# Optimization experiments

Measured on AMD Instinct MI355X. Metric: run time of the kernel, lower is better.

Reference implementation:

```python
import jax, jax.numpy as jnp
import numpy as np

BATCH, SEQ, DIM, DSTATE = 8, 2048, 1024, 16


def setup_inputs() -> dict:
    key = jax.random.key(0)
    ks = jax.random.split(key, 8)
    u = jax.random.normal(ks[0], (BATCH, SEQ, DIM), jnp.float32)
    gate = jax.random.normal(ks[1], (BATCH, SEQ, DIM), jnp.float32)
    # parameters (init per module: normal std=0.01 for A_log/B/C, zeros for D)
    A_log = 0.01 * jax.random.normal(ks[2], (DSTATE, DSTATE), jnp.float32)
    B_mat = 0.01 * jax.random.normal(ks[3], (DIM, DSTATE), jnp.float32)
    C_mat = 0.01 * jax.random.normal(ks[4], (DIM, DSTATE), jnp.float32)
    D = jnp.zeros((DIM,), jnp.float32)
    bound = 1.0 / np.sqrt(DIM)  # nn.Linear default init
    dt_w = jax.random.uniform(ks[5], (1, DIM), jnp.float32, -bound, bound)
    dt_b = jax.random.uniform(ks[6], (1,), jnp.float32, -bound, bound)
    return {"u": u, "gate": gate, "A_log": A_log, "B_mat": B_mat,
            "C_mat": C_mat, "D": D, "dt_w": dt_w, "dt_b": dt_b}


def reference(u, gate, A_log, B_mat, C_mat, D, dt_w, dt_b):
    # delta = sigmoid(Linear(gate)) : [B, S, 1] -> [B, S]
    delta = jax.nn.sigmoid(jnp.einsum('bsd,od->bso', gate, dt_w) + dt_b)[..., 0]
    A = -jnp.exp(A_log)                               # [N, N]
    scaled_A = delta[..., None, None] * A             # [B, S, N, N]
    A_exp = jax.scipy.linalg.expm(scaled_A)           # batched matrix exp
    Bu = jnp.einsum('bsd,dn->bsn', u, B_mat)          # [B, S, N]

    def step(h, inp):
        Aexp_t, bu_t = inp                            # [B,N,N], [B,N]
        h = jnp.einsum('bn,bnm->bm', h, Aexp_t) + bu_t
        return h, h

    h0 = jnp.zeros((u.shape[0], DSTATE), u.dtype)
    _, hs = jax.lax.scan(step, h0, (jnp.swapaxes(A_exp, 0, 1), jnp.swapaxes(Bu, 0, 1)))
    hs = jnp.swapaxes(hs, 0, 1)                       # [B, S, N]
    y = jnp.einsum('bsn,dn->bsd', hs, C_mat) + D * u  # [B, S, D]
    return y
```

## Files before the change

kernel.cpp:

```cpp
#include <hip/hip_runtime.h>

#define BATCH  8
#define SEQ    2048
#define DIMSZ  1024
#define NST    16
#define LCH    32
#define CPB    (SEQ / LCH)
#define NCHUNK (BATCH * CPB)
#define NCHEB  32
#define PI_F   3.14159265358979f

typedef __attribute__((ext_vector_type(8))) short bf16x8;
typedef __attribute__((ext_vector_type(4))) float f32x4;

static __device__ __forceinline__ unsigned short f2bf(float f) {
    unsigned u = __builtin_bit_cast(unsigned, f);
    unsigned r = (u + 0x7FFFu + ((u >> 16) & 1u)) >> 16;
    return (unsigned short)r;
}
static __device__ __forceinline__ float bf2f(unsigned short h) {
    unsigned u = ((unsigned)h) << 16;
    return __builtin_bit_cast(float, u);
}

__global__ __launch_bounds__(256) void sA_nodes(
    const float* __restrict__ A_log, float* __restrict__ Fn)
{
    __shared__ float Xs[16 * 17];
    __shared__ float Ts[16 * 17];
    const int tid = threadIdx.x;
    const int i = tid >> 4, j = tid & 15;
    const float th = (2.f * blockIdx.x + 1.f) * (PI_F / 64.f);
    const float dl = 0.5f * (1.f + cosf(th));
    const float a  = -expf(A_log[tid]);
    const float x  = dl * a * (1.0f / 64.0f);
    Xs[i*17 + j] = x;
    Ts[i*17 + j] = x;
    float S = x + (i == j ? 1.0f : 0.0f);
    __syncthreads();
#pragma unroll
    for (int k = 2; k <= 8; ++k) {
        float nt = 0.f;
#pragma unroll
        for (int kk = 0; kk < 16; ++kk)
            nt = fmaf(Ts[i*17 + kk], Xs[kk*17 + j], nt);
        nt *= (1.0f / (float)k);
        S += nt;
        __syncthreads();
        Ts[i*17 + j] = nt;
        __syncthreads();
    }
#pragma unroll
    for (int r = 0; r < 6; ++r) {
        __syncthreads();
        Ts[i*17 + j] = S;
        __syncthreads();
        float nt = 0.f;
#pragma unroll
        for (int kk = 0; kk < 16; ++kk)
            nt = fmaf(Ts[i*17 + kk], Ts[kk*17 + j], nt);
        S = nt;
    }
    Fn[(size_t)blockIdx.x * 256 + tid] = S;
}

__global__ __launch_bounds__(256) void sB_setup(
    const float* __restrict__ Fn, const float* __restrict__ B_mat,
    float* __restrict__ Gt,
    unsigned short* __restrict__ Bfh, unsigned short* __restrict__ Bfl)
{
    const int tid = threadIdx.x;
    const int blk = blockIdx.x;
    if (blk < NCHEB) {
        const int m = blk;
        float acc = 0.f;
        for (int k = 0; k < NCHEB; ++k) {
            const float th = (2.f * k + 1.f) * (PI_F / 64.f);
            acc = fmaf(Fn[(size_t)k * 256 + tid], cosf(m * th), acc);
        }
        const float sc = (m == 0) ? (1.f / 32.f) : (2.f / 32.f);
        Gt[(size_t)tid * NCHEB + m] = acc * sc;
    } else {
        const int idx0 = (blk - NCHEB) * 2048;
        for (int t = 0; t < 8; ++t) {
            const int idx = idx0 + t * 256 + tid;
            const int j  = idx & 7;
            const int l  = (idx >> 3) & 63;
            const int ks = idx >> 9;
            const int k  = ks * 32 + ((l >> 4) << 3) + j;
            const int n  = l & 15;
            float bv = B_mat[(size_t)k * 16 + n];
            unsigned short h = f2bf(bv);
            Bfh[idx] = h;
            Bfl[idx] = f2bf(bv - bf2f(h));
        }
    }
}

__global__ __launch_bounds__(256) void k1a_delta(
    const float* __restrict__ gate, const float* __restrict__ dt_w,
    const float* __restrict__ dt_b, float* __restrict__ delta)
{
    const int tid  = threadIdx.x;
    const int lane = tid & 63;
    const int w    = tid >> 6;
    const int tok  = blockIdx.x * 4 + w;
    const float* gp = gate + (size_t)tok * DIMSZ;
    float s = 0.f;
#pragma unroll
    for (int i = 0; i < 4; ++i) {
        const float4 g  = *(const float4*)(gp   + i * 256 + lane * 4);
        const float4 wv = *(const float4*)(dt_w + i * 256 + lane * 4);
        s = fmaf(g.x, wv.x, s); s = fmaf(g.y, wv.y, s);
        s = fmaf(g.z, wv.z, s); s = fmaf(g.w, wv.w, s);
    }
#pragma unroll
    for (int off = 32; off >= 1; off >>= 1)
        s += __shfl_xor(s, off, 64);
    if (lane == 0)
        delta[tok] = 1.0f / (1.0f + expf(-(s + dt_b[0])));
}

__global__ __launch_bounds__(512, 4) void kBA2(
    const float* __restrict__ u,
    const unsigned short* __restrict__ Bfh, const unsigned short* __restrict__ Bfl,
    const float* __restrict__ Gt, const float* __restrict__ delta,
    float* __restrict__ Bu, float* __restrict__ P, float* __restrict__ e)
{
    __shared__ float smem[12288];
    __shared__ float Bus[LCH * NST];
    __shared__ float dl[LCH];
    __shared__ float sd[1];
    __shared__ float Ps[16 * 17];
    const int tid  = threadIdx.x;
    const int lane = tid & 63;
    const int w    = tid >> 6;
    const size_t gI = blockIdx.x;
    const int tok0 = (int)gI * 32;
    const int qk   = w & 3;
    const int wrow = (w >> 2) * 16;
    const int q    = lane >> 4;
    const int r    = lane & 15;

    if (tid < LCH) dl[tid] = delta[gI * LCH + tid];

    const uint4* bh = (const uint4*)Bfh;
    const uint4* bl = (const uint4*)Bfl;

    const int srow = 4 * w + (lane >> 5);
    const int p    = lane & 31;
    int colb[2];
#pragma unroll
    for (int i = 0; i < 2; ++i) {
        const int row = srow + 2 * i;
        colb[i] = 256 * (p >> 3) + 4 * ((p & 7) ^ (row & 7));
    }

    auto stage = [&](int c, int b) {
#pragma unroll
        for (int i = 0; i < 2; ++i) {
            const float* gp = u + (size_t)(tok0 + srow + 2 * i) * DIMSZ
                                + (colb[i] + c * 32);
            __builtin_amdgcn_global_load_lds(
                (const __attribute__((address_space(1))) void*)gp,
                (__attribute__((address_space(3))) void*)&smem[b * 4096 + (4 * w + 2 * i) * 128],
                16, 0, 0);
        }
    };

    f32x4 acc = {0.f, 0.f, 0.f, 0.f};
    uint4 fh[2], fl[2];

    fh[0] = bh[(qk * 8 + 0) * 64 + lane];
    fl[0] = bl[(qk * 8 + 0) * 64 + lane];
    stage(0, 0);
    stage(1, 1);
    stage(2, 2);
    asm volatile("s_waitcnt vmcnt(4)" ::: "memory");
    __builtin_amdgcn_sched_barrier(0);
    __builtin_amdgcn_s_barrier();

#pragma unroll
    for (int c = 0; c < 8; ++c) {
        const int b = c % 3;
        float fu[8];
        {
            const int c0 = qk * 8 + ((2 * q + 0) ^ (r & 7));
            const int c1 = qk * 8 + ((2 * q + 1) ^ (r & 7));
            const float4 v0 = *(const float4*)&smem[b * 4096 + (wrow + r) * 128 + c0 * 4];
            const float4 v1 = *(const float4*)&smem[b * 4096 + (wrow + r) * 128 + c1 * 4];
            fu[0] = v0.x; fu[1] = v0.y; fu[2] = v0.z; fu[3] = v0.w;
            fu[4] = v1.x; fu[5] = v1.y; fu[6] = v1.z; fu[7] = v1.w;
        }
        asm volatile("s_waitcnt lgkmcnt(0)" ::: "memory");
        __builtin_amdgcn_sched_barrier(0);
        __builtin_amdgcn_s_barrier();
        if (c + 1 < 8) {
            const int ks = qk * 8 + c + 1;
            fh[(c + 1) & 1] = bh[ks * 64 + lane];
            fl[(c + 1) & 1] = bl[ks * 64 + lane];
        }
        if (c + 3 < 8) stage(c + 3, (c + 3) % 3);
        __builtin_amdgcn_sched_barrier(0);
        {
            bf16x8 uh, ul;
#pragma unroll
            for (int i = 0; i < 8; ++i) {
                unsigned short h = f2bf(fu[i]);
                uh[i] = (short)h;
                ul[i] = (short)f2bf(fu[i] - bf2f(h));
            }
            const bf16x8 Bh = __builtin_bit_cast(bf16x8, fh[c & 1]);
            const bf16x8 Bl = __builtin_bit_cast(bf16x8, fl[c & 1]);
            acc = __builtin_amdgcn_mfma_f32_16x16x32_bf16(uh, Bh, acc, 0, 0, 0);
            acc = __builtin_amdgcn_mfma_f32_16x16x32_bf16(uh, Bl, acc, 0, 0, 0);
            acc = __builtin_amdgcn_mfma_f32_16x16x32_bf16(ul, Bh, acc, 0, 0, 0);
        }
        if (c < 7) {
            if (c == 6) asm volatile("s_waitcnt vmcnt(4)" ::: "memory");
            else        asm volatile("s_waitcnt vmcnt(6)" ::: "memory");
            __builtin_amdgcn_sched_barrier(0);
            __builtin_amdgcn_s_barrier();
        }
    }

    float* red = smem;
#pragma unroll
    for (int rr = 0; rr < 4; ++rr)
        red[w * 256 + (q * 4 + rr) * 16 + r] = acc[rr];
    __syncthreads();
    float bv;
    if (tid < 256) bv = red[tid]       + red[256 + tid] + red[512 + tid]  + red[768 + tid];
    else           bv = red[768 + tid] + red[1024 + tid] + red[1280 + tid] + red[1536 + tid];
    Bu[gI * 512 + tid] = bv;
    Bus[tid] = bv;

    const int el = tid & 255;
    float gr[NCHEB];
    {
        const float4* gp = (const float4*)(Gt + (size_t)el * NCHEB);
#pragma unroll
        for (int qq = 0; qq < NCHEB / 4; ++qq) {
            float4 v = gp[qq];
            gr[qq*4+0] = v.x; gr[qq*4+1] = v.y; gr[qq*4+2] = v.z; gr[qq*4+3] = v.w;
        }
    }
    __syncthreads();
    if (tid == 0) {
        float s = 0.f;
        for (int t = 0; t < LCH; ++t) s += dl[t];
        sd[0] = s;
    }
    const int tgrp = tid >> 8;
    for (int t = tgrp * 16; t < tgrp * 16 + 16; ++t) {
        const float x = 2.f * dl[t] - 1.f;
        float accm = fmaf(gr[1], x, gr[0]);
        float tm2 = 1.f, tm1 = x;
#pragma unroll
        for (int m = 2; m < NCHEB; ++m) {
            const float tm = fmaf(2.f * x, tm1, -tm2);
            accm = fmaf(gr[m], tm, accm);
            tm2 = tm1; tm1 = tm;
        }
        smem[t * 272 + (el >> 4) * 17 + (el & 15)] = accm;
    }
    __syncthreads();
    float S;
    {
        const float xp = 2.f * (sd[0] * (1.f / LCH)) - 1.f;
        float accm = fmaf(gr[1], xp, gr[0]);
        float tm2 = 1.f, tm1 = xp;
#pragma unroll
        for (int m = 2; m < NCHEB; ++m) {
            const float tm = fmaf(2.f * xp, tm1, -tm2);
            accm = fmaf(gr[m], tm, accm);
            tm2 = tm1; tm1 = tm;
        }
        S = accm;
    }
    const int i = el >> 4, j = el & 15;
#pragma unroll
    for (int rr = 0; rr < 5; ++rr) {
        if (tid < 256) Ps[i*17 + j] = S;
        __syncthreads();
        float ns = 0.f;
#pragma unroll
        for (int k = 0; k < 16; ++k)
            ns = fmaf(Ps[i*17 + k], Ps[k*17 + j], ns);
        __syncthreads();
        S = ns;
    }
    if (tid < 256) P[gI * 256 + tid] = S;
    if (tid < 64) {
        const int gq = tid >> 4, jj = tid & 15, i0 = gq * 4;
        float h = 0.f;
        for (int t = 0; t < LCH; ++t) {
            float pp = 0.f;
#pragma unroll
            for (int m = 0; m < 4; ++m)
                pp = fmaf(__shfl(h, gq * 20 + m, 64),
                          smem[t * 272 + (i0 + m) * 17 + jj], pp);
            pp += __shfl_xor(pp, 16, 64);
            pp += __shfl_xor(pp, 32, 64);
            h = Bus[t * 16 + jj] + pp;
        }
        if (gq == 0) e[gI * NST + jj] = h;
    }
}

__global__ __launch_bounds__(256) void k4_scan(
    const float* __restrict__ P, const float* __restrict__ e,
    float* __restrict__ hin)
{
    __shared__ float Pl[32 * 272];
    __shared__ float el[32 * NST];
    const int tid = threadIdx.x;
    const int b = blockIdx.x;
    float h = 0.f;
    for (int half = 0; half < 2; ++half) {
        const int c0 = half * 32;
        for (int idx = tid; idx < 32*256; idx += 256) {
            const int c = idx >> 8, ij = idx & 255, i = ij >> 4, jj = ij & 15;
            Pl[c*272 + i*17 + jj] = P[((size_t)(b*CPB + c0 + c)) * 256 + ij];
        }
        for (int idx = tid; idx < 32*NST; idx += 256)
            el[idx] = e[((size_t)(b*CPB + c0)) * NST + idx];
        __syncthreads();
        if (tid < 64) {
            const int gq = tid >> 4, j = tid & 15, i0 = gq * 4;
            for (int c = 0; c < 32; ++c) {
                if (tid < 16) hin[((size_t)(b*CPB + c0 + c)) * NST + j] = h;
                float pp = 0.f;
#pragma unroll
                for (int m = 0; m < 4; ++m)
                    pp = fmaf(__shfl(h, gq * 20 + m, 64),
                              Pl[c*272 + (i0 + m)*17 + j], pp);
                pp += __shfl_xor(pp, 16, 64);
                pp += __shfl_xor(pp, 32, 64);
                h = el[c*16 + j] + pp;
            }
        }
        __syncthreads();
    }
}

__global__ __launch_bounds__(512, 4) void k5b(
    const float* __restrict__ Gt, const float* __restrict__ delta,
    const float* __restrict__ Bu, const float* __restrict__ hin,
    const float* __restrict__ u, const float* __restrict__ C_mat,
    const float* __restrict__ D, float* __restrict__ y)
{
    __shared__ float Mlds[32 * 272];
    __shared__ float Bus[LCH * NST];
    __shared__ float dl[LCH];
    __shared__ __align__(16) float Hs[LCH * NST];
    const int tid = threadIdx.x;
    const size_t g = blockIdx.x;
    const int el = tid & 255;
    const int tgrp = tid >> 8;
    if (tid < LCH) dl[tid] = delta[g * LCH + tid];
    Bus[tid] = Bu[g * 512 + tid];
    float gr[NCHEB];
    {
        const float4* gp = (const float4*)(Gt + (size_t)el * NCHEB);
#pragma unroll
        for (int qq = 0; qq < NCHEB / 4; ++qq) {
            float4 v = gp[qq];
            gr[qq*4+0] = v.x; gr[qq*4+1] = v.y; gr[qq*4+2] = v.z; gr[qq*4+3] = v.w;
        }
    }
    __syncthreads();
    for (int t = tgrp * 16; t < tgrp * 16 + 16; ++t) {
        const float x = 2.f * dl[t] - 1.f;
        float accm = fmaf(gr[1], x, gr[0]);
        float tm2 = 1.f, tm1 = x;
#pragma unroll
        for (int m = 2; m < NCHEB; ++m) {
            const float tm = fmaf(2.f * x, tm1, -tm2);
            accm = fmaf(gr[m], tm, accm);
            tm2 = tm1; tm1 = tm;
        }
        Mlds[t * 272 + (el >> 4) * 17 + (el & 15)] = accm;
    }
    __syncthreads();
    if (tid < 64) {
        const int gq = tid >> 4, jj = tid & 15, i0 = gq * 4;
        float h = hin[g * NST + jj];
        for (int t = 0; t < LCH; ++t) {
            float pp = 0.f;
#pragma unroll
            for (int m = 0; m < 4; ++m)
                pp = fmaf(__shfl(h, gq * 20 + m, 64),
                          Mlds[t * 272 + (i0 + m) * 17 + jj], pp);
            pp += __shfl_xor(pp, 16, 64);
            pp += __shfl_xor(pp, 32, 64);
            h = Bus[t * 16 + jj] + pp;
            if (gq == 0) Hs[t * 16 + jj] = h;
        }
    }
    __syncthreads();
    const int d0 = el * 4;
    float4 cr[4][4];
#pragma unroll
    for (int r = 0; r < 4; ++r)
#pragma unroll
        for (int qq = 0; qq < 4; ++qq)
            cr[r][qq] = ((const float4*)C_mat)[(d0 + r) * 4 + qq];
    const float4 dv = ((const float4*)D)[el];
    const bool dnz = (dv.x != 0.f) || (dv.y != 0.f) || (dv.z != 0.f) || (dv.w != 0.f);
    for (int t = tgrp * 16; t < tgrp * 16 + 16; ++t) {
        const size_t row = (g * LCH + t) * DIMSZ;
        float y0 = 0.f, y1 = 0.f, y2 = 0.f, y3 = 0.f;
        if (dnz) {
            const float4 uv = ((const float4*)(u + row))[el];
            y0 = dv.x * uv.x; y1 = dv.y * uv.y; y2 = dv.z * uv.z; y3 = dv.w * uv.w;
        }
#pragma unroll
        for (int qq = 0; qq < 4; ++qq) {
            const float4 hq = *((const float4*)&Hs[t*16 + qq*4]);
            y0 = fmaf(hq.x, cr[0][qq].x, y0); y0 = fmaf(hq.y, cr[0][qq].y, y0);
            y0 = fmaf(hq.z, cr[0][qq].z, y0); y0 = fmaf(hq.w, cr[0][qq].w, y0);
            y1 = fmaf(hq.x, cr[1][qq].x, y1); y1 = fmaf(hq.y, cr[1][qq].y, y1);
            y1 = fmaf(hq.z, cr[1][qq].z, y1); y1 = fmaf(hq.w, cr[1][qq].w, y1);
            y2 = fmaf(hq.x, cr[2][qq].x, y2); y2 = fmaf(hq.y, cr[2][qq].y, y2);
            y2 = fmaf(hq.z, cr[2][qq].z, y2); y2 = fmaf(hq.w, cr[2][qq].w, y2);
            y3 = fmaf(hq.x, cr[3][qq].x, y3); y3 = fmaf(hq.y, cr[3][qq].y, y3);
            y3 = fmaf(hq.z, cr[3][qq].z, y3); y3 = fmaf(hq.w, cr[3][qq].w, y3);
        }
        float4 ov; ov.x = y0; ov.y = y1; ov.z = y2; ov.w = y3;
        ((float4*)(y + row))[el] = ov;
    }
}

extern "C" void kernel_launch(void* const* d_in, const int* in_sizes, int n_in,
                              void* d_out, int out_size, void* d_ws, size_t ws_size,
                              hipStream_t stream)
{
    const float* u     = (const float*)d_in[0];
    const float* gate  = (const float*)d_in[1];
    const float* A_log = (const float*)d_in[2];
    const float* B_mat = (const float*)d_in[3];
    const float* C_mat = (const float*)d_in[4];
    const float* D     = (const float*)d_in[5];
    const float* dt_w  = (const float*)d_in[6];
    const float* dt_b  = (const float*)d_in[7];
    float* y = (float*)d_out;

    float* ws = (float*)d_ws;
    size_t o = 0;
    float* Fn    = ws + o; o += 32 * 256;
    float* Gt    = ws + o; o += 256 * NCHEB;
    float* delta = ws + o; o += (size_t)BATCH * SEQ;
    float* Bu    = ws + o; o += (size_t)BATCH * SEQ * NST;
    float* P     = ws + o; o += (size_t)NCHUNK * 256;
    float* e     = ws + o; o += (size_t)NCHUNK * NST;
    float* hin   = ws + o; o += (size_t)NCHUNK * NST;
    unsigned short* Bfh = (unsigned short*)(ws + o); o += 8192;
    unsigned short* Bfl = (unsigned short*)(ws + o); o += 8192;

    sA_nodes <<<NCHEB,     256, 0, stream>>>(A_log, Fn);
    sB_setup <<<NCHEB + 8, 256, 0, stream>>>(Fn, B_mat, Gt, Bfh, Bfl);
    k1a_delta<<<BATCH * SEQ / 4, 256, 0, stream>>>(gate, dt_w, dt_b, delta);
    kBA2     <<<NCHUNK,    512, 0, stream>>>(u, Bfh, Bfl, Gt, delta, Bu, P, e);
    k4_scan  <<<BATCH,     256, 0, stream>>>(P, e, hin);
    k5b      <<<NCHUNK,    512, 0, stream>>>(Gt, delta, Bu, hin, u, C_mat, D, y);
}
```

Measured before the change: 249.3 us.

## Replace LDS-staged u pipeline with direct global loads; shrink output kernel to 256 threads

The Bu projection kernel drops its triple-buffered global_load_lds staging, swizzled LDS reads and per-step barriers. Each lane now loads its u fragment and B fragments straight from global memory into registers before the split-bf16 MFMAs. The LDS buffer shrinks and the launch-bounds occupancy hint falls from 4 to 2. The output kernel moves from 512 to 256 threads per block, so each thread handles all 32 timesteps instead of splitting them across two halves. This removes barrier and LDS traffic, but gives up explicit latency hiding and puts less parallelism in each block of the output stage.

```diff
diff --git a/kernel.cpp b/kernel.cpp
--- a/kernel.cpp
+++ b/kernel.cpp
@@ -121,13 +121,13 @@
         delta[tok] = 1.0f / (1.0f + expf(-(s + dt_b[0])));
 }
 
-__global__ __launch_bounds__(512, 4) void kBA2(
+__global__ __launch_bounds__(512, 2) void kBA3(
     const float* __restrict__ u,
     const unsigned short* __restrict__ Bfh, const unsigned short* __restrict__ Bfl,
     const float* __restrict__ Gt, const float* __restrict__ delta,
     float* __restrict__ Bu, float* __restrict__ P, float* __restrict__ e)
 {
-    __shared__ float smem[12288];
+    __shared__ float smem[8704];
     __shared__ float Bus[LCH * NST];
     __shared__ float dl[LCH];
     __shared__ float sd[1];
@@ -138,7 +138,7 @@
     const size_t gI = blockIdx.x;
     const int tok0 = (int)gI * 32;
     const int qk   = w & 3;
-    const int wrow = (w >> 2) * 16;
+    const int tt   = w >> 2;
     const int q    = lane >> 4;
     const int r    = lane & 15;
 
@@ -147,81 +147,28 @@
     const uint4* bh = (const uint4*)Bfh;
     const uint4* bl = (const uint4*)Bfl;
 
-    const int srow = 4 * w + (lane >> 5);
-    const int p    = lane & 31;
-    int colb[2];
-#pragma unroll
-    for (int i = 0; i < 2; ++i) {
-        const int row = srow + 2 * i;
-        colb[i] = 256 * (p >> 3) + 4 * ((p & 7) ^ (row & 7));
-    }
-
-    auto stage = [&](int c, int b) {
-#pragma unroll
-        for (int i = 0; i < 2; ++i) {
-            const float* gp = u + (size_t)(tok0 + srow + 2 * i) * DIMSZ
-                                + (colb[i] + c * 32);
-            __builtin_amdgcn_global_load_lds(
-                (const __attribute__((address_space(1))) void*)gp,
-                (__attribute__((address_space(3))) void*)&smem[b * 4096 + (4 * w + 2 * i) * 128],
-                16, 0, 0);
-        }
-    };
+    const float* up = u + (size_t)(tok0 + tt * 16 + r) * DIMSZ + qk * 256 + q * 8;
 
     f32x4 acc = {0.f, 0.f, 0.f, 0.f};
-    uint4 fh[2], fl[2];
-
-    fh[0] = bh[(qk * 8 + 0) * 64 + lane];
-    fl[0] = bl[(qk * 8 + 0) * 64 + lane];
-    stage(0, 0);
-    stage(1, 1);
-    stage(2, 2);
-    asm volatile("s_waitcnt vmcnt(4)" ::: "memory");
-    __builtin_amdgcn_sched_barrier(0);
-    __builtin_amdgcn_s_barrier();
-
 #pragma unroll
     for (int c = 0; c < 8; ++c) {
-        const int b = c % 3;
-        float fu[8];
-        {
-            const int c0 = qk * 8 + ((2 * q + 0) ^ (r & 7));
-            const int c1 = qk * 8 + ((2 * q + 1) ^ (r & 7));
-            const float4 v0 = *(const float4*)&smem[b * 4096 + (wrow + r) * 128 + c0 * 4];
-            const float4 v1 = *(const float4*)&smem[b * 4096 + (wrow + r) * 128 + c1 * 4];
-            fu[0] = v0.x; fu[1] = v0.y; fu[2] = v0.z; fu[3] = v0.w;
-            fu[4] = v1.x; fu[5] = v1.y; fu[6] = v1.z; fu[7] = v1.w;
-        }
-        asm volatile("s_waitcnt lgkmcnt(0)" ::: "memory");
-        __builtin_amdgcn_sched_barrier(0);
-        __builtin_amdgcn_s_barrier();
-        if (c + 1 < 8) {
-            const int ks = qk * 8 + c + 1;
-            fh[(c + 1) & 1] = bh[ks * 64 + lane];
-            fl[(c + 1) & 1] = bl[ks * 64 + lane];
-        }
-        if (c + 3 < 8) stage(c + 3, (c + 3) % 3);
-        __builtin_amdgcn_sched_barrier(0);
-        {
-            bf16x8 uh, ul;
-#pragma unroll
-            for (int i = 0; i < 8; ++i) {
-                unsigned short h = f2bf(fu[i]);
-                uh[i] = (short)h;
-                ul[i] = (short)f2bf(fu[i] - bf2f(h));
-            }
-            const bf16x8 Bh = __builtin_bit_cast(bf16x8, fh[c & 1]);
-            const bf16x8 Bl = __builtin_bit_cast(bf16x8, fl[c & 1]);
-            acc = __builtin_amdgcn_mfma_f32_16x16x32_bf16(uh, Bh, acc, 0, 0, 0);
-            acc = __builtin_amdgcn_mfma_f32_16x16x32_bf16(uh, Bl, acc, 0, 0, 0);
-            acc = __builtin_amdgcn_mfma_f32_16x16x32_bf16(ul, Bh, acc, 0, 0, 0);
-        }
-        if (c < 7) {
-            if (c == 6) asm volatile("s_waitcnt vmcnt(4)" ::: "memory");
-            else        asm volatile("s_waitcnt vmcnt(6)" ::: "memory");
-            __builtin_amdgcn_sched_barrier(0);
-            __builtin_amdgcn_s_barrier();
-        }
+        const float4 v0 = *(const float4*)(up + c * 32);
+        const float4 v1 = *(const float4*)(up + c * 32 + 4);
+        const uint4 FH = bh[(qk * 8 + c) * 64 + lane];
+        const uint4 FL = bl[(qk * 8 + c) * 64 + lane];
+        const float fu[8] = {v0.x, v0.y, v0.z, v0.w, v1.x, v1.y, v1.z, v1.w};
+        bf16x8 uh, ul;
+#pragma unroll
+        for (int i = 0; i < 8; ++i) {
+            unsigned short h = f2bf(fu[i]);
+            uh[i] = (short)h;
+            ul[i] = (short)f2bf(fu[i] - bf2f(h));
+        }
+        const bf16x8 Bh = __builtin_bit_cast(bf16x8, FH);
+        const bf16x8 Bl = __builtin_bit_cast(bf16x8, FL);
+        acc = __builtin_amdgcn_mfma_f32_16x16x32_bf16(uh, Bh, acc, 0, 0, 0);
+        acc = __builtin_amdgcn_mfma_f32_16x16x32_bf16(uh, Bl, acc, 0, 0, 0);
+        acc = __builtin_amdgcn_mfma_f32_16x16x32_bf16(ul, Bh, acc, 0, 0, 0);
     }
 
     float* red = smem;
@@ -229,9 +176,8 @@
     for (int rr = 0; rr < 4; ++rr)
         red[w * 256 + (q * 4 + rr) * 16 + r] = acc[rr];
     __syncthreads();
-    float bv;
-    if (tid < 256) bv = red[tid]       + red[256 + tid] + red[512 + tid]  + red[768 + tid];
-    else           bv = red[768 + tid] + red[1024 + tid] + red[1280 + tid] + red[1536 + tid];
+    const int rb = (tid >> 8) * 1024 + (tid & 255);
+    const float bv = red[rb] + red[rb + 256] + red[rb + 512] + red[rb + 768];
     Bu[gI * 512 + tid] = bv;
     Bus[tid] = bv;
 
@@ -344,7 +290,7 @@
     }
 }
 
-__global__ __launch_bounds__(512, 4) void k5b(
+__global__ __launch_bounds__(256) void k5_out(
     const float* __restrict__ Gt, const float* __restrict__ delta,
     const float* __restrict__ Bu, const float* __restrict__ hin,
     const float* __restrict__ u, const float* __restrict__ C_mat,
@@ -356,13 +302,12 @@
     __shared__ __align__(16) float Hs[LCH * NST];
     const int tid = threadIdx.x;
     const size_t g = blockIdx.x;
-    const int el = tid & 255;
-    const int tgrp = tid >> 8;
     if (tid < LCH) dl[tid] = delta[g * LCH + tid];
-    Bus[tid] = Bu[g * 512 + tid];
+    for (int idx = tid; idx < LCH * NST; idx += 256)
+        Bus[idx] = Bu[g * (size_t)(LCH * NST) + idx];
     float gr[NCHEB];
     {
-        const float4* gp = (const float4*)(Gt + (size_t)el * NCHEB);
+        const float4* gp = (const float4*)(Gt + (size_t)tid * NCHEB);
 #pragma unroll
         for (int qq = 0; qq < NCHEB / 4; ++qq) {
             float4 v = gp[qq];
@@ -370,7 +315,7 @@
         }
     }
     __syncthreads();
-    for (int t = tgrp * 16; t < tgrp * 16 + 16; ++t) {
+    for (int t = 0; t < LCH; ++t) {
         const float x = 2.f * dl[t] - 1.f;
         float accm = fmaf(gr[1], x, gr[0]);
         float tm2 = 1.f, tm1 = x;
@@ -380,7 +325,7 @@
             accm = fmaf(gr[m], tm, accm);
             tm2 = tm1; tm1 = tm;
         }
-        Mlds[t * 272 + (el >> 4) * 17 + (el & 15)] = accm;
+        Mlds[t * 272 + (tid >> 4) * 17 + (tid & 15)] = accm;
     }
     __syncthreads();
     if (tid < 64) {
@@ -399,20 +344,20 @@
         }
     }
     __syncthreads();
-    const int d0 = el * 4;
+    const int d0 = tid * 4;
     float4 cr[4][4];
 #pragma unroll
     for (int r = 0; r < 4; ++r)
 #pragma unroll
         for (int qq = 0; qq < 4; ++qq)
             cr[r][qq] = ((const float4*)C_mat)[(d0 + r) * 4 + qq];
-    const float4 dv = ((const float4*)D)[el];
+    const float4 dv = ((const float4*)D)[tid];
     const bool dnz = (dv.x != 0.f) || (dv.y != 0.f) || (dv.z != 0.f) || (dv.w != 0.f);
-    for (int t = tgrp * 16; t < tgrp * 16 + 16; ++t) {
+    for (int t = 0; t < LCH; ++t) {
         const size_t row = (g * LCH + t) * DIMSZ;
         float y0 = 0.f, y1 = 0.f, y2 = 0.f, y3 = 0.f;
         if (dnz) {
-            const float4 uv = ((const float4*)(u + row))[el];
+            const float4 uv = ((const float4*)(u + row))[tid];
             y0 = dv.x * uv.x; y1 = dv.y * uv.y; y2 = dv.z * uv.z; y3 = dv.w * uv.w;
         }
 #pragma unroll
@@ -428,7 +373,7 @@
             y3 = fmaf(hq.z, cr[3][qq].z, y3); y3 = fmaf(hq.w, cr[3][qq].w, y3);
         }
         float4 ov; ov.x = y0; ov.y = y1; ov.z = y2; ov.w = y3;
-        ((float4*)(y + row))[el] = ov;
+        ((float4*)(y + row))[tid] = ov;
     }
 }
 
@@ -461,7 +406,7 @@
     sA_nodes <<<NCHEB,     256, 0, stream>>>(A_log, Fn);
     sB_setup <<<NCHEB + 8, 256, 0, stream>>>(Fn, B_mat, Gt, Bfh, Bfl);
     k1a_delta<<<BATCH * SEQ / 4, 256, 0, stream>>>(gate, dt_w, dt_b, delta);
-    kBA2     <<<NCHUNK,    512, 0, stream>>>(u, Bfh, Bfl, Gt, delta, Bu, P, e);
+    kBA3     <<<NCHUNK,    512, 0, stream>>>(u, Bfh, Bfl, Gt, delta, Bu, P, e);
     k4_scan  <<<BATCH,     256, 0, stream>>>(P, e, hin);
-    k5b      <<<NCHUNK,    512, 0, stream>>>(Gt, delta, Bu, hin, u, C_mat, D, y);
-}
+    k5_out   <<<NCHUNK,    256, 0, stream>>>(Gt, delta, Bu, hin, u, C_mat, D, y);
+}
```

Result: no change. 251.1 us (+0.7%).
